# Kernel optimization log

Measured on AMD Instinct MI355X. Metric: run time of the kernel, lower is better.

## Reference

```python
import jax, jax.numpy as jnp
import numpy as np

L, H, P = 16384, 1024, 512
DT_MIN, DT_MAX = 1e-3, 1e-1
STEP_RESCALE = 1.0


def setup_inputs() -> dict:
    key = jax.random.key(0)
    ks = jax.random.split(key, 7)
    input_sequence = jax.random.normal(ks[0], (L, H), jnp.float32)
    # eigenvalues with negative real part (left half plane), HiPPO-like imag parts
    Lambda_re = -(jax.random.uniform(ks[1], (P,), jnp.float32) * 0.9 + 0.1)
    Lambda_im = jnp.pi * jnp.arange(P, dtype=jnp.float32)
    B = jax.random.normal(ks[2], (P, H, 2), jnp.float32) / jnp.sqrt(2.0 * H)   # real/imag of B_tilde (P,H)
    C = jax.random.normal(ks[3], (H, P, 2), jnp.float32) / jnp.sqrt(2.0 * P)   # real/imag of C_tilde (H,P)
    D = jax.random.normal(ks[4], (H,), jnp.float32)
    u01 = jax.random.uniform(ks[5], (P, 1), jnp.float32)
    log_step = jnp.log(DT_MIN) + u01 * (jnp.log(DT_MAX) - jnp.log(DT_MIN))     # (P,1)
    return dict(input_sequence=input_sequence, Lambda_re=Lambda_re, Lambda_im=Lambda_im,
                B=B, C=C, D=D, log_step=log_step)


def _binop(q_i, q_j):
    # diagonal linear recurrence composition: (A, b) pairs
    A_i, b_i = q_i
    A_j, b_j = q_j
    return A_j * A_i, A_j * b_i + b_j


def reference(input_sequence, Lambda_re, Lambda_im, B, C, D, log_step):
    Lambda = Lambda_re + 1j * Lambda_im                        # (P,) complex64
    B_tilde = B[..., 0] + 1j * B[..., 1]                       # (P,H)
    C_tilde = C[..., 0] + 1j * C[..., 1]                       # (H,P)
    step = STEP_RESCALE * jnp.exp(log_step[:, 0])              # (P,)
    # ZOH discretization
    Lambda_bar = jnp.exp(Lambda * step)                        # (P,)
    B_bar = ((Lambda_bar - 1.0) / Lambda)[:, None] * B_tilde   # (P,H)
    # Bu_elements: (L,P) complex
    Bu = input_sequence.astype(B_bar.dtype) @ B_bar.T
    Lambda_elems = jnp.broadcast_to(Lambda_bar, Bu.shape)      # (L,P)
    # parallel associative scan over the diagonal recurrence x_t = Lambda_bar*x_{t-1} + Bu_t
    _, xs = jax.lax.associative_scan(_binop, (Lambda_elems, Bu))
    ys = 2.0 * (xs @ C_tilde.T).real                           # conj_sym => factor 2, (L,H)
    return ys + D * input_sequence
```

## Files before the change

kernel.cpp:

```cpp
#include <hip/hip_runtime.h>
#include <math.h>

#define L_SEQ 16384
#define H_DIM 1024
#define P_DIM 512
#define N2P   1024
#define KDIM  1024
#define NKT   16
#define CHUNK 64
#define NCHUNK 256

typedef __attribute__((ext_vector_type(8))) short short8;
typedef __attribute__((ext_vector_type(4))) float f32x4;

__device__ __forceinline__ unsigned short f2bf(float f){
    unsigned int u = __float_as_uint(f);
    u = (u + 0x7FFFu + ((u >> 16) & 1u)) >> 16;
    return (unsigned short)u;
}
__device__ __forceinline__ float bf2f(unsigned int lo16){
    return __uint_as_float(lo16 << 16);
}

__global__ void k_prep_lambda(const float* __restrict__ lre, const float* __restrict__ lim,
                              const float* __restrict__ lstep,
                              float* __restrict__ lam, float* __restrict__ coef,
                              float* __restrict__ lpow)
{
    int p = threadIdx.x;
    double step = exp((double)lstep[p]);
    double dr = (double)lre[p], di = (double)lim[p];
    double ar = dr*step, ai = di*step;
    double er = exp(ar);
    double lbr = er*cos(ai), lbi = er*sin(ai);
    lam[2*p] = (float)lbr; lam[2*p+1] = (float)lbi;
    double nr = lbr - 1.0, ni = lbi;
    double d2 = dr*dr + di*di;
    coef[2*p]   = (float)((nr*dr + ni*di)/d2);
    coef[2*p+1] = (float)((ni*dr - nr*di)/d2);
    double xr = lbr, xi = lbi;
    #pragma unroll
    for (int s=0;s<6;s++){ double t = xr*xr - xi*xi; xi = 2.0*xr*xi; xr = t; }
    lpow[2*p] = (float)xr; lpow[2*p+1] = (float)xi;
}

__global__ __launch_bounds__(256)
void k_prep_BB(const float* __restrict__ B, const float* __restrict__ coef,
               unsigned short* __restrict__ BB)
{
    int i = blockIdx.x*256 + threadIdx.x;
    int p = i >> 10, h = i & 1023;
    float br = B[2*i], bi = B[2*i+1];
    float cr = coef[2*p], ci = coef[2*p+1];
    BB[(size_t)(2*p)*H_DIM + h]   = f2bf(cr*br - ci*bi);
    BB[(size_t)(2*p+1)*H_DIM + h] = f2bf(cr*bi + ci*br);
}

__global__ __launch_bounds__(256)
void k_prep_CC(const float* __restrict__ C, unsigned short* __restrict__ CC)
{
    int i = blockIdx.x*256 + threadIdx.x;
    int h = i >> 9, p = i & 511;
    float cr = C[2*i], ci = C[2*i+1];
    CC[(size_t)h*N2P + 2*p]     = f2bf(2.f*cr);
    CC[(size_t)h*N2P + 2*p + 1] = f2bf(-2.f*ci);
}

__global__ __launch_bounds__(256)
void k_cast(const float4* __restrict__ u, unsigned short* __restrict__ o)
{
    int i = blockIdx.x*256 + threadIdx.x;
    float4 a = u[2*i], b = u[2*i+1];
    union { short8 v; unsigned short s[8]; } r;
    r.s[0]=f2bf(a.x); r.s[1]=f2bf(a.y); r.s[2]=f2bf(a.z); r.s[3]=f2bf(a.w);
    r.s[4]=f2bf(b.x); r.s[5]=f2bf(b.y); r.s[6]=f2bf(b.z); r.s[7]=f2bf(b.w);
    *reinterpret_cast<short8*>(o + (size_t)i*8) = r.v;
}

template<int EPI>
__global__ __launch_bounds__(512, 2)
void gemm256(const unsigned short* __restrict__ A, const unsigned short* __restrict__ Bm,
             float* __restrict__ Cf, unsigned short* __restrict__ Cb,
             const float* __restrict__ Dv, const unsigned short* __restrict__ U16)
{
    __shared__ char lds[131072];
    const int tid  = threadIdx.x;
    const int lane = tid & 63;
    const int wid  = tid >> 6;
    const int wm = wid >> 2, wn = wid & 3;
    const int wg = ((int)blockIdx.x & 7) * 32 + ((int)blockIdx.x >> 3);
    const int tm = wg >> 2, tn = wg & 3;
    const int lr = lane & 15;

    const int scol = ((tid & 7) ^ ((tid >> 3) & 7)) << 3;
    const int srow = tid >> 3;
    const int kc0 = (((lane >> 4)      ^ (lr & 7)) << 4);
    const int kc1 = ((((lane >> 4) | 4) ^ (lr & 7)) << 4);
    const int aSub = wm*16384 + lr*128;
    const int bSub = 32768 + (wn >> 1)*16384 + (wn & 1)*8192 + lr*128;

#define GLOAD(SRC, DST) __builtin_amdgcn_global_load_lds( \
        (const __attribute__((address_space(1))) void*)(SRC), \
        (__attribute__((address_space(3))) void*)(DST), 16, 0, 0)
#define STAGE_A(kt_, h_) do{ \
    char* d_ = lds + (((kt_)&1)<<16) + (h_)*16384 + tid*16; \
    const unsigned short* s_ = A + (size_t)(tm*256 + (h_)*128 + srow)*KDIM + (size_t)(kt_)*64 + scol; \
    GLOAD(s_, d_); GLOAD(s_ + (size_t)64*KDIM, d_ + 8192); }while(0)
#define STAGE_B(kt_, h_) do{ \
    char* d_ = lds + (((kt_)&1)<<16) + 32768 + (h_)*16384 + tid*16; \
    const unsigned short* s_ = Bm + (size_t)(tn*256 + (h_)*128 + srow)*KDIM + (size_t)(kt_)*64 + scol; \
    GLOAD(s_, d_); GLOAD(s_ + (size_t)64*KDIM, d_ + 8192); }while(0)
#define RD(OFF) (*(const short8*)(lds + (OFF)))
#define MFMA(a,b,c) __builtin_amdgcn_mfma_f32_16x16x32_bf16(a,b,c,0,0,0)
#define VMC0  asm volatile("s_waitcnt vmcnt(0)" ::: "memory")
#define ABAR  asm volatile("s_barrier" ::: "memory")

    f32x4 acc[8][4];
    #pragma unroll
    for (int m=0;m<8;m++)
        #pragma unroll
        for (int n=0;n<4;n++) acc[m][n] = (f32x4){0.f,0.f,0.f,0.f};

    STAGE_A(0,0); STAGE_A(0,1); STAGE_B(0,0); STAGE_B(0,1);
    VMC0; ABAR;

    #pragma unroll 2
    for (int kt = 0; kt < NKT; ++kt) {
        const int sb = (kt & 1) << 16;
        const int tN = (kt+1 < NKT) ? kt+1 : NKT-1;
        STAGE_A(tN, 0); STAGE_A(tN, 1); STAGE_B(tN, 0); STAGE_B(tN, 1);

        #pragma unroll
        for (int ks=0; ks<2; ++ks){
            const int kc = ks ? kc1 : kc0;
            short8 bfr[4];
            #pragma unroll
            for (int n=0;n<4;n++) bfr[n] = RD(sb + bSub + n*2048 + kc);
            #pragma unroll
            for (int mh=0; mh<2; ++mh){
                short8 afr[4];
                #pragma unroll
                for (int m=0;m<4;m++) afr[m] = RD(sb + aSub + (mh*4+m)*2048 + kc);
                #pragma unroll
                for (int m=0;m<4;m++)
                    #pragma unroll
                    for (int n=0;n<4;n++)
                        acc[mh*4+m][n] = MFMA(afr[m], bfr[n], acc[mh*4+m][n]);
            }
        }
        VMC0;
        ABAR;
    }

    const int orow0 = tm*256 + wm*128 + (lane>>4)*4;
    const int ocol0 = tn*256 + wn*64 + lr;
    #pragma unroll
    for (int m=0;m<8;m++){
        #pragma unroll
        for (int n=0;n<4;n++){
            int row = orow0 + m*16, col = ocol0 + n*16;
            #pragma unroll
            for (int j=0;j<4;j++){
                size_t idx = (size_t)(row + j)*N2P + col;
                if (EPI) Cf[idx] = acc[m][n][j] + Dv[col]*bf2f(U16[idx]);
                else     Cb[idx] = f2bf(acc[m][n][j]);
            }
        }
    }
#undef GLOAD
#undef STAGE_A
#undef STAGE_B
#undef RD
#undef MFMA
#undef VMC0
#undef ABAR
}

__global__ __launch_bounds__(512)
void k_agg(const unsigned int* __restrict__ Bu, const float* __restrict__ lam,
           float* __restrict__ agg)
{
    int p = threadIdx.x, c = blockIdx.x;
    float lrr = lam[2*p], lii = lam[2*p+1];
    float xr = 0.f, xi = 0.f;
    const unsigned int* b2 = Bu + (size_t)c*CHUNK*512 + p;
    #pragma unroll 4
    for (int t=0;t<CHUNK;t++){
        unsigned int b = b2[(size_t)t*512];
        float br = __uint_as_float(b << 16);
        float bi = __uint_as_float(b & 0xffff0000u);
        float tr = lrr*xr - lii*xi + br;
        xi = lrr*xi + lii*xr + bi;
        xr = tr;
    }
    agg[((size_t)c*P_DIM + p)*2]     = xr;
    agg[((size_t)c*P_DIM + p)*2 + 1] = xi;
}

__global__ __launch_bounds__(256)
void k_scan(const float* __restrict__ agg, const float* __restrict__ lpow,
            float* __restrict__ xinit)
{
    __shared__ float sr[NCHUNK], si[NCHUNK];
    int c = threadIdx.x, p = blockIdx.x;
    float xr = agg[((size_t)c*P_DIM + p)*2];
    float xi = agg[((size_t)c*P_DIM + p)*2 + 1];
    sr[c] = xr; si[c] = xi;
    float wr = lpow[2*p], wi = lpow[2*p+1];
    for (int s=1; s<NCHUNK; s<<=1){
        __syncthreads();
        float ur = 0.f, ui = 0.f;
        if (c >= s){ ur = sr[c-s]; ui = si[c-s]; }
        __syncthreads();
        xr += wr*ur - wi*ui;
        xi += wr*ui + wi*ur;
        sr[c] = xr; si[c] = xi;
        float t = wr*wr - wi*wi; wi = 2.f*wr*wi; wr = t;
    }
    __syncthreads();
    float er = 0.f, ei = 0.f;
    if (c > 0){ er = sr[c-1]; ei = si[c-1]; }
    xinit[((size_t)c*P_DIM + p)*2]     = er;
    xinit[((size_t)c*P_DIM + p)*2 + 1] = ei;
}

__global__ __launch_bounds__(512)
void k_apply(const unsigned int* __restrict__ Bu, const float* __restrict__ lam,
             const float* __restrict__ xinit, unsigned int* __restrict__ xs)
{
    int p = threadIdx.x, c = blockIdx.x;
    float lrr = lam[2*p], lii = lam[2*p+1];
    float xr = xinit[((size_t)c*P_DIM + p)*2];
    float xi = xinit[((size_t)c*P_DIM + p)*2 + 1];
    const unsigned int* b2 = Bu + (size_t)c*CHUNK*512 + p;
    unsigned int* o = xs + (size_t)c*CHUNK*512 + p;
    #pragma unroll 4
    for (int t=0;t<CHUNK;t++){
        unsigned int b = b2[(size_t)t*512];
        float br = __uint_as_float(b << 16);
        float bi = __uint_as_float(b & 0xffff0000u);
        float tr = lrr*xr - lii*xi + br;
        xi = lrr*xi + lii*xr + bi;
        xr = tr;
        o[(size_t)t*512] = (unsigned int)f2bf(xr) | ((unsigned int)f2bf(xi) << 16);
    }
}

extern "C" void kernel_launch(void* const* d_in, const int* in_sizes, int n_in,
                              void* d_out, int out_size, void* d_ws, size_t ws_size,
                              hipStream_t stream)
{
    const float* u   = (const float*)d_in[0];
    const float* lre = (const float*)d_in[1];
    const float* lim = (const float*)d_in[2];
    const float* B   = (const float*)d_in[3];
    const float* C   = (const float*)d_in[4];
    const float* D   = (const float*)d_in[5];
    const float* ls  = (const float*)d_in[6];
    float* out = (float*)d_out;

    char* w = (char*)d_ws;
    unsigned short* u16  = (unsigned short*)(w + 0);
    unsigned short* xs16 = (unsigned short*)(w + 33554432);
    unsigned short* Bu16 = (unsigned short*)(w + 67108864);
    unsigned short* BB   = (unsigned short*)(w + 100663296);
    unsigned short* CC   = (unsigned short*)(w + 102760448);
    float* lam   = (float*)(w + 104857600);
    float* coef  = (float*)(w + 104861696);
    float* lpow  = (float*)(w + 104865792);
    float* agg   = (float*)(w + 104869888);
    float* xinit = (float*)(w + 105918464);

    k_prep_lambda<<<1, P_DIM, 0, stream>>>(lre, lim, ls, lam, coef, lpow);
    k_prep_BB<<<(P_DIM*H_DIM)/256, 256, 0, stream>>>(B, coef, BB);
    k_prep_CC<<<(H_DIM*P_DIM)/256, 256, 0, stream>>>(C, CC);
    k_cast<<<(L_SEQ*H_DIM)/(256*8), 256, 0, stream>>>((const float4*)u, u16);

    gemm256<0><<<256, 512, 0, stream>>>(u16, BB, nullptr, Bu16, nullptr, nullptr);

    k_agg<<<NCHUNK, P_DIM, 0, stream>>>((const unsigned int*)Bu16, lam, agg);
    k_scan<<<P_DIM, NCHUNK, 0, stream>>>(agg, lpow, xinit);
    k_apply<<<NCHUNK, P_DIM, 0, stream>>>((const unsigned int*)Bu16, lam, xinit,
                                          (unsigned int*)xs16);

    gemm256<1><<<256, 512, 0, stream>>>(xs16, CC, out, nullptr, D, u16);
}
```

Baseline: 131.1 us.

## Shrink GEMM tiles to 128x128 and load B fragments directly from global

Replaces the 256x256-tile, 512-thread GEMM with a 128x128-tile, 256-thread kernel launched on 1024 blocks, cutting LDS per block from 128KB to 32KB so more blocks fit per CU. The B operand is no longer staged through LDS; each wave reads its B fragments directly from global memory (relying on cache), and only A is double-buffered in LDS. This trades per-tile data reuse and coalesced B staging for higher occupancy and a fuller grid across the 256 CUs, at the risk of more global/L2 traffic and exposed B load latency.

```diff
diff --git a/kernel.cpp b/kernel.cpp
--- a/kernel.cpp
+++ b/kernel.cpp
@@ -78,84 +78,91 @@
 }
 
 template<int EPI>
-__global__ __launch_bounds__(512, 2)
-void gemm256(const unsigned short* __restrict__ A, const unsigned short* __restrict__ Bm,
+__global__ __launch_bounds__(256, 3)
+void gemm128(const unsigned short* __restrict__ A, const unsigned short* __restrict__ Bm,
              float* __restrict__ Cf, unsigned short* __restrict__ Cb,
              const float* __restrict__ Dv, const unsigned short* __restrict__ U16)
 {
-    __shared__ char lds[131072];
+    __shared__ char lds[32768];
     const int tid  = threadIdx.x;
     const int lane = tid & 63;
     const int wid  = tid >> 6;
-    const int wm = wid >> 2, wn = wid & 3;
-    const int wg = ((int)blockIdx.x & 7) * 32 + ((int)blockIdx.x >> 3);
-    const int tm = wg >> 2, tn = wg & 3;
+    const int wm = wid >> 1, wn = wid & 1;
+    const int wg = ((int)blockIdx.x & 7) * 128 + ((int)blockIdx.x >> 3);
+    const int tm = wg >> 3, tn = wg & 7;
     const int lr = lane & 15;
 
+    const int srow = tid >> 3;
     const int scol = ((tid & 7) ^ ((tid >> 3) & 7)) << 3;
-    const int srow = tid >> 3;
     const int kc0 = (((lane >> 4)      ^ (lr & 7)) << 4);
     const int kc1 = ((((lane >> 4) | 4) ^ (lr & 7)) << 4);
-    const int aSub = wm*16384 + lr*128;
-    const int bSub = 32768 + (wn >> 1)*16384 + (wn & 1)*8192 + lr*128;
+    const int aOff = (wm*64 + lr)*128;
+
+    const unsigned short* bP = Bm + (size_t)(tn*128 + wn*64 + lr)*KDIM + ((lane >> 4) << 3);
 
 #define GLOAD(SRC, DST) __builtin_amdgcn_global_load_lds( \
         (const __attribute__((address_space(1))) void*)(SRC), \
         (__attribute__((address_space(3))) void*)(DST), 16, 0, 0)
-#define STAGE_A(kt_, h_) do{ \
-    char* d_ = lds + (((kt_)&1)<<16) + (h_)*16384 + tid*16; \
-    const unsigned short* s_ = A + (size_t)(tm*256 + (h_)*128 + srow)*KDIM + (size_t)(kt_)*64 + scol; \
-    GLOAD(s_, d_); GLOAD(s_ + (size_t)64*KDIM, d_ + 8192); }while(0)
-#define STAGE_B(kt_, h_) do{ \
-    char* d_ = lds + (((kt_)&1)<<16) + 32768 + (h_)*16384 + tid*16; \
-    const unsigned short* s_ = Bm + (size_t)(tn*256 + (h_)*128 + srow)*KDIM + (size_t)(kt_)*64 + scol; \
-    GLOAD(s_, d_); GLOAD(s_ + (size_t)64*KDIM, d_ + 8192); }while(0)
+#define STAGE_A(kt_) do{ \
+    char* d_ = lds + (((kt_)&1)<<14) + tid*16; \
+    const unsigned short* s_ = A + (size_t)(tm*128 + srow)*KDIM + (size_t)(kt_)*64 + scol; \
+    GLOAD(s_,                    d_); \
+    GLOAD(s_ + (size_t)32*KDIM,  d_ + 4096); \
+    GLOAD(s_ + (size_t)64*KDIM,  d_ + 8192); \
+    GLOAD(s_ + (size_t)96*KDIM,  d_ + 12288); }while(0)
 #define RD(OFF) (*(const short8*)(lds + (OFF)))
 #define MFMA(a,b,c) __builtin_amdgcn_mfma_f32_16x16x32_bf16(a,b,c,0,0,0)
 #define VMC0  asm volatile("s_waitcnt vmcnt(0)" ::: "memory")
 #define ABAR  asm volatile("s_barrier" ::: "memory")
 
-    f32x4 acc[8][4];
+    f32x4 acc[4][4];
     #pragma unroll
-    for (int m=0;m<8;m++)
+    for (int m=0;m<4;m++)
         #pragma unroll
         for (int n=0;n<4;n++) acc[m][n] = (f32x4){0.f,0.f,0.f,0.f};
 
-    STAGE_A(0,0); STAGE_A(0,1); STAGE_B(0,0); STAGE_B(0,1);
+    STAGE_A(0);
     VMC0; ABAR;
 
     #pragma unroll 2
     for (int kt = 0; kt < NKT; ++kt) {
-        const int sb = (kt & 1) << 16;
+        const int sb = (kt & 1) << 14;
         const int tN = (kt+1 < NKT) ? kt+1 : NKT-1;
-        STAGE_A(tN, 0); STAGE_A(tN, 1); STAGE_B(tN, 0); STAGE_B(tN, 1);
-
+        STAGE_A(tN);
+
+        const unsigned short* bK = bP + (size_t)kt*64;
+        short8 b0[4], b1[4];
         #pragma unroll
-        for (int ks=0; ks<2; ++ks){
-            const int kc = ks ? kc1 : kc0;
-            short8 bfr[4];
-            #pragma unroll
-            for (int n=0;n<4;n++) bfr[n] = RD(sb + bSub + n*2048 + kc);
-            #pragma unroll
-            for (int mh=0; mh<2; ++mh){
-                short8 afr[4];
+        for (int n=0;n<4;n++){
+            b0[n] = *reinterpret_cast<const short8*>(bK + n*16*KDIM);
+            b1[n] = *reinterpret_cast<const short8*>(bK + n*16*KDIM + 32);
+        }
+        {
+            short8 afr[4];
+            #pragma unroll
+            for (int m=0;m<4;m++) afr[m] = RD(sb + aOff + m*2048 + kc0);
+            #pragma unroll
+            for (int m=0;m<4;m++)
                 #pragma unroll
-                for (int m=0;m<4;m++) afr[m] = RD(sb + aSub + (mh*4+m)*2048 + kc);
+                for (int n=0;n<4;n++) acc[m][n] = MFMA(afr[m], b0[n], acc[m][n]);
+        }
+        {
+            short8 afr[4];
+            #pragma unroll
+            for (int m=0;m<4;m++) afr[m] = RD(sb + aOff + m*2048 + kc1);
+            #pragma unroll
+            for (int m=0;m<4;m++)
                 #pragma unroll
-                for (int m=0;m<4;m++)
-                    #pragma unroll
-                    for (int n=0;n<4;n++)
-                        acc[mh*4+m][n] = MFMA(afr[m], bfr[n], acc[mh*4+m][n]);
-            }
+                for (int n=0;n<4;n++) acc[m][n] = MFMA(afr[m], b1[n], acc[m][n]);
         }
         VMC0;
         ABAR;
     }
 
-    const int orow0 = tm*256 + wm*128 + (lane>>4)*4;
-    const int ocol0 = tn*256 + wn*64 + lr;
+    const int orow0 = tm*128 + wm*64 + (lane>>4)*4;
+    const int ocol0 = tn*128 + wn*64 + lr;
     #pragma unroll
-    for (int m=0;m<8;m++){
+    for (int m=0;m<4;m++){
         #pragma unroll
         for (int n=0;n<4;n++){
             int row = orow0 + m*16, col = ocol0 + n*16;
@@ -169,7 +176,6 @@
     }
 #undef GLOAD
 #undef STAGE_A
-#undef STAGE_B
 #undef RD
 #undef MFMA
 #undef VMC0
@@ -276,12 +282,12 @@
     k_prep_CC<<<(H_DIM*P_DIM)/256, 256, 0, stream>>>(C, CC);
     k_cast<<<(L_SEQ*H_DIM)/(256*8), 256, 0, stream>>>((const float4*)u, u16);
 
-    gemm256<0><<<256, 512, 0, stream>>>(u16, BB, nullptr, Bu16, nullptr, nullptr);
+    gemm128<0><<<1024, 256, 0, stream>>>(u16, BB, nullptr, Bu16, nullptr, nullptr);
 
     k_agg<<<NCHUNK, P_DIM, 0, stream>>>((const unsigned int*)Bu16, lam, agg);
     k_scan<<<P_DIM, NCHUNK, 0, stream>>>(agg, lpow, xinit);
     k_apply<<<NCHUNK, P_DIM, 0, stream>>>((const unsigned int*)Bu16, lam, xinit,
                                           (unsigned int*)xs16);
 
-    gemm256<1><<<256, 512, 0, stream>>>(xs16, CC, out, nullptr, D, u16);
-}
+    gemm128<1><<<1024, 256, 0, stream>>>(xs16, CC, out, nullptr, D, u16);
+}
```

Result: slower. 201.5 us (+53.7%).
